# Performance work log

Hardware: AMD Instinct MI355X
Metric: run time of the kernel (lower is better)

Reference implementation:

```python
import jax, jax.numpy as jnp
import numpy as np

N = 50000      # n_nodes
E = 600000     # n_edges (avg degree 12)
IN_DIM = 128
HID = 256
OUT = 2


def _glorot(k, fan_in, fan_out):
    s = jnp.sqrt(6.0 / (fan_in + fan_out))
    return jax.random.uniform(k, (fan_in, fan_out), jnp.float32, -s, s)


def setup_inputs() -> dict:
    key = jax.random.key(0)
    ks = jax.random.split(key, 6)
    x = jax.random.normal(ks[0], (N, IN_DIM), jnp.float32)
    edge_index = jax.random.randint(ks[1], (2, E), 0, N, jnp.int32)
    W1 = _glorot(ks[2], IN_DIM, HID)
    b1 = jnp.zeros((HID,), jnp.float32)
    W2 = _glorot(ks[3], HID, HID)
    b2 = jnp.zeros((HID,), jnp.float32)
    Wl = _glorot(ks[4], HID, OUT)
    bl = jnp.zeros((OUT,), jnp.float32)
    return {"x": x, "edge_index": edge_index, "W1": W1, "b1": b1,
            "W2": W2, "b2": b2, "Wl": Wl, "bl": bl}


def _gcn_conv(x, W, b, src, dst, dinv, n):
    # PyG GCNConv: transform, then propagate with symmetric norm + self-loops.
    h = x @ W                                   # [N, F_out]
    norm = (dinv[src] * dinv[dst])[:, None]     # [E, 1]
    agg = jax.ops.segment_sum(h[src] * norm, dst, num_segments=n)
    agg = agg + h * (dinv * dinv)[:, None]      # self-loop term: deg^-1 * h
    return agg + b


def reference(x, edge_index, W1, b1, W2, b2, Wl, bl):
    n = x.shape[0]
    src, dst = edge_index[0], edge_index[1]
    # degree (with self-loop) computed on destination nodes, as in PyG gcn_norm
    deg = jax.ops.segment_sum(jnp.ones((src.shape[0],), jnp.float32), dst,
                              num_segments=n) + 1.0
    dinv = jax.lax.rsqrt(deg)
    h = jax.nn.relu(_gcn_conv(x, W1, b1, src, dst, dinv, n))
    # dropout is identity in eval mode
    h = jax.nn.relu(_gcn_conv(h, W2, b2, src, dst, dinv, n))
    return h @ Wl + bl
```

## Files before the change

### kernel.cpp

```cpp
#include <hip/hip_runtime.h>
#include <hip/hip_bf16.h>
#include <hip/hip_fp16.h>

constexpr int IN_DIM = 128;
constexpr int HID    = 256;

typedef _Float16 f16x8 __attribute__((ext_vector_type(8)));
typedef float    f32x4 __attribute__((ext_vector_type(4)));


__global__ void count_deg(const int* __restrict__ dst, int* __restrict__ deg, int e) {
    int i = blockIdx.x * blockDim.x + threadIdx.x;
    if (i < e) atomicAdd(&deg[dst[i]], 1);
}

__global__ __launch_bounds__(256) void scan_partial(const int* __restrict__ deg,
                                                    int* __restrict__ escan,
                                                    int* __restrict__ blocksum,
                                                    float* __restrict__ dinv, int n) {
    __shared__ int lds[256];
    int t = threadIdx.x;
    int i = blockIdx.x * 256 + t;
    int v = (i < n) ? deg[i] : 0;
    if (i < n) dinv[i] = rsqrtf((float)v + 1.0f);
    lds[t] = v;
    __syncthreads();
    for (int off = 1; off < 256; off <<= 1) {
        int a = lds[t];
        int w = (t >= off) ? lds[t - off] : 0;
        __syncthreads();
        lds[t] = a + w;
        __syncthreads();
    }
    if (i < n) escan[i] = lds[t] - v;
    if (t == 255) blocksum[blockIdx.x] = lds[255];
}

__global__ __launch_bounds__(256) void scan_rest(const int* __restrict__ escan,
                                                 const int* __restrict__ blocksum,
                                                 int nb, int* __restrict__ rowptr, int n) {
    __shared__ int lds[256];
    int t = threadIdx.x;
    int v = (t < nb) ? blocksum[t] : 0;
    lds[t] = v;
    __syncthreads();
    for (int off = 1; off < 256; off <<= 1) {
        int a = lds[t];
        int w = (t >= off) ? lds[t - off] : 0;
        __syncthreads();
        lds[t] = a + w;
        __syncthreads();
    }
    int boff = (blockIdx.x > 0) ? lds[blockIdx.x - 1] : 0;
    int i = blockIdx.x * 256 + t;
    if (i < n) rowptr[i] = escan[i] + boff;
    if (blockIdx.x == 0 && t == 0) rowptr[n] = lds[nb - 1];
}

__global__ void scatter_edges(const int* __restrict__ src, const int* __restrict__ dst,
                              const int* __restrict__ rowptr, int* __restrict__ cursor,
                              const float* __restrict__ dinv,
                              int2* __restrict__ esw, int e) {
    int i = blockIdx.x * blockDim.x + threadIdx.x;
    if (i < e) {
        int d = dst[i];
        int s = src[i];
        int p = atomicAdd(&cursor[d], 1);
        esw[rowptr[d] + p] = make_int2(s, __float_as_int(dinv[s] * dinv[d]));
    }
}

__device__ inline void conv_B_elem(const float* B, ushort* Bp, int id) {
    int k  = id >> 6;
    int n4 = (id & 63) * 4;
    float4 v = *(const float4*)(B + (size_t)k * 256 + n4);
    size_t base = (size_t)(k >> 5) * (256 * 32) + (k & 31);
    Bp[base + (size_t)(n4 + 0) * 32] = __half_as_ushort(__float2half(v.x));
    Bp[base + (size_t)(n4 + 1) * 32] = __half_as_ushort(__float2half(v.y));
    Bp[base + (size_t)(n4 + 2) * 32] = __half_as_ushort(__float2half(v.z));
    Bp[base + (size_t)(n4 + 3) * 32] = __half_as_ushort(__float2half(v.w));
}

__global__ void convert_inputs(const float* __restrict__ W1, ushort* __restrict__ B1p,
                               const float* __restrict__ W2, ushort* __restrict__ B2p,
                               const float* __restrict__ x, ushort* __restrict__ xh,
                               int total4, int* __restrict__ deg,
                               int* __restrict__ cursor, int n) {
    int id = blockIdx.x * 256 + threadIdx.x;
    constexpr int C1 = IN_DIM * 64;
    constexpr int C2 = C1 + HID * 64;
    if (id < C1) {
        conv_B_elem(W1, B1p, id);
    } else if (id < C2) {
        conv_B_elem(W2, B2p, id - C1);
    } else if (id < C2 + total4) {
        int i = id - C2;
        float4 v = *(const float4*)(x + (size_t)i * 4);
        ushort4 o;
        o.x = __half_as_ushort(__float2half(v.x));
        o.y = __half_as_ushort(__float2half(v.y));
        o.z = __half_as_ushort(__float2half(v.z));
        o.w = __half_as_ushort(__float2half(v.w));
        *(ushort4*)(xh + (size_t)i * 4) = o;
    } else {
        int i = id - (C2 + total4);
        if (i < n) { deg[i] = 0; cursor[i] = 0; }
    }
}

template <int K>
__global__ __launch_bounds__(256) void aggregate_p(const ushort* __restrict__ h,
                                                   const int* __restrict__ rowptr,
                                                   const int2* __restrict__ esw,
                                                   const float* __restrict__ dinv,
                                                   ushort* __restrict__ Pp,
                                                   int n, int Mp) {
    constexpr int VH = K / 64;
    int wid  = (blockIdx.x * 256 + threadIdx.x) >> 6;
    int lane = threadIdx.x & 63;
    if (wid >= n) return;
    float di = dinv[wid];
    float sw = di * di;
    float acc[VH];
    {
        const ushort* row = h + (size_t)wid * K + lane * VH;
        if constexpr (VH == 4) {
            uint2 u = *(const uint2*)row;
            float2 fa = __half22float2(*(__half2*)&u.x);
            float2 fb = __half22float2(*(__half2*)&u.y);
            acc[0] = fa.x * sw; acc[1] = fa.y * sw; acc[2] = fb.x * sw; acc[3] = fb.y * sw;
        } else {
            uint u = *(const uint*)row;
            float2 fa = __half22float2(*(__half2*)&u);
            acc[0] = fa.x * sw; acc[1] = fa.y * sw;
        }
    }
    int beg = rowptr[wid], fin = rowptr[wid + 1];
    for (int b = beg; b < fin; b += 64) {
        int cnt = fin - b;
        if (cnt > 64) cnt = 64;
        int2 pk = (lane < cnt) ? esw[b + lane] : make_int2(0, 0);
        int   sv = pk.x;
        float wv = __int_as_float(pk.y);
        int t = 0;
        for (; t + 8 <= cnt; t += 8) {
            float wr[8];
            if constexpr (VH == 4) {
                uint2 u[8];
#pragma unroll
                for (int k = 0; k < 8; k++) {
                    int s = __shfl(sv, t + k);
                    wr[k] = __shfl(wv, t + k);
                    u[k] = *(const uint2*)(h + (size_t)s * K + lane * VH);
                }
#pragma unroll
                for (int k = 0; k < 8; k++) {
                    float2 fa = __half22float2(*(__half2*)&u[k].x);
                    float2 fb = __half22float2(*(__half2*)&u[k].y);
                    acc[0] += fa.x * wr[k]; acc[1] += fa.y * wr[k];
                    acc[2] += fb.x * wr[k]; acc[3] += fb.y * wr[k];
                }
            } else {
                uint u[8];
#pragma unroll
                for (int k = 0; k < 8; k++) {
                    int s = __shfl(sv, t + k);
                    wr[k] = __shfl(wv, t + k);
                    u[k] = *(const uint*)(h + (size_t)s * K + lane * VH);
                }
#pragma unroll
                for (int k = 0; k < 8; k++) {
                    float2 fa = __half22float2(*(__half2*)&u[k]);
                    acc[0] += fa.x * wr[k]; acc[1] += fa.y * wr[k];
                }
            }
        }
        for (; t + 4 <= cnt; t += 4) {
            float wr[4];
            if constexpr (VH == 4) {
                uint2 u[4];
#pragma unroll
                for (int k = 0; k < 4; k++) {
                    int s = __shfl(sv, t + k);
                    wr[k] = __shfl(wv, t + k);
                    u[k] = *(const uint2*)(h + (size_t)s * K + lane * VH);
                }
#pragma unroll
                for (int k = 0; k < 4; k++) {
                    float2 fa = __half22float2(*(__half2*)&u[k].x);
                    float2 fb = __half22float2(*(__half2*)&u[k].y);
                    acc[0] += fa.x * wr[k]; acc[1] += fa.y * wr[k];
                    acc[2] += fb.x * wr[k]; acc[3] += fb.y * wr[k];
                }
            } else {
                uint u[4];
#pragma unroll
                for (int k = 0; k < 4; k++) {
                    int s = __shfl(sv, t + k);
                    wr[k] = __shfl(wv, t + k);
                    u[k] = *(const uint*)(h + (size_t)s * K + lane * VH);
                }
#pragma unroll
                for (int k = 0; k < 4; k++) {
                    float2 fa = __half22float2(*(__half2*)&u[k]);
                    acc[0] += fa.x * wr[k]; acc[1] += fa.y * wr[k];
                }
            }
        }
        for (; t < cnt; t++) {
            int   s = __shfl(sv, t);
            float w = __shfl(wv, t);
            const ushort* r = h + (size_t)s * K + lane * VH;
            if constexpr (VH == 4) {
                uint2 u = *(const uint2*)r;
                float2 fa = __half22float2(*(__half2*)&u.x);
                float2 fb = __half22float2(*(__half2*)&u.y);
                acc[0] += fa.x * w; acc[1] += fa.y * w;
                acc[2] += fb.x * w; acc[3] += fb.y * w;
            } else {
                uint u = *(const uint*)r;
                float2 fa = __half22float2(*(__half2*)&u);
                acc[0] += fa.x * w; acc[1] += fa.y * w;
            }
        }
    }
    int kglob = lane * VH;
    int chunk = kglob >> 5;
    int inner = kglob & 31;
    size_t base = (size_t)chunk * Mp * 32 + (size_t)wid * 32 + inner;
    if constexpr (VH == 4) {
        __half2 p0 = __floats2half2_rn(acc[0], acc[1]);
        __half2 p1 = __floats2half2_rn(acc[2], acc[3]);
        *(uint2*)&Pp[base] = make_uint2(*(uint*)&p0, *(uint*)&p1);
    } else {
        __half2 p0 = __floats2half2_rn(acc[0], acc[1]);
        *(uint*)&Pp[base] = *(uint*)&p0;
    }
}

template <int K, int MODE>
__global__ __launch_bounds__(256, 3) void gemm_f16(const ushort* __restrict__ Ap,
                                                   const ushort* __restrict__ Bp,
                                                   const float* __restrict__ bias,
                                                   ushort* __restrict__ C16,
                                                   const float* __restrict__ Wl,
                                                   const float* __restrict__ bl,
                                                   float* __restrict__ out,
                                                   int M, int Mp) {
    constexpr int NC = K / 32;
    __shared__ ushort Asm[NC * 1024];
    __shared__ ushort Bsm[2][8192];
    __shared__ float part[4][32][2];

    int tid  = threadIdx.x;
    int w    = tid >> 6;
    int lane = tid & 63;
    int l15  = lane & 15;
    int quad = lane >> 4;
    int row0 = blockIdx.x * 32;

    constexpr int TOTA = NC * 2;
    for (int j = w; j < TOTA; j += 4) {
        int c   = j >> 1;
        int sub = j & 1;
        const ushort* g = Ap + (size_t)c * Mp * 32 + (size_t)(row0 + sub * 16) * 32;
        ushort* l = Asm + c * 1024 + sub * 512;
        __builtin_amdgcn_global_load_lds(
            (const __attribute__((address_space(1))) uint*)(g + (size_t)lane * 8),
            (__attribute__((address_space(3))) uint*)l, 16, 0, 0);
    }
#pragma unroll
    for (int j = 0; j < 4; j++) {
        int seg = w * 4 + j;
        const ushort* g = Bp + (size_t)seg * 512;
        ushort* l = Bsm[0] + seg * 512;
        __builtin_amdgcn_global_load_lds(
            (const __attribute__((address_space(1))) uint*)(g + (size_t)lane * 8),
            (__attribute__((address_space(3))) uint*)l, 16, 0, 0);
    }

    f32x4 acc[2][4] = {};
#pragma unroll
    for (int c = 0; c < NC; c++) {
        __syncthreads();
        if (c + 1 < NC) {
            int nb_ = (c + 1) & 1;
#pragma unroll
            for (int j = 0; j < 4; j++) {
                int seg = w * 4 + j;
                const ushort* g = Bp + (size_t)(c + 1) * 8192 + (size_t)seg * 512;
                ushort* l = Bsm[nb_] + seg * 512;
                __builtin_amdgcn_global_load_lds(
                    (const __attribute__((address_space(1))) uint*)(g + (size_t)lane * 8),
                    (__attribute__((address_space(3))) uint*)l, 16, 0, 0);
            }
        }
        f16x8 fa[2], fb[4];
#pragma unroll
        for (int i = 0; i < 2; i++) {
            int off = c * 1024 + (i * 16 + l15) * 32 + quad * 8;
            fa[i] = *(const f16x8*)&Asm[off];
        }
#pragma unroll
        for (int j = 0; j < 4; j++) {
            int off = (w * 64 + j * 16 + l15) * 32 + quad * 8;
            fb[j] = *(const f16x8*)&Bsm[c & 1][off];
        }
#pragma unroll
        for (int i = 0; i < 2; i++)
#pragma unroll
            for (int j = 0; j < 4; j++)
                acc[i][j] = __builtin_amdgcn_mfma_f32_16x16x32_f16(fa[i], fb[j], acc[i][j], 0, 0, 0);
    }

    float bj[4];
#pragma unroll
    for (int j = 0; j < 4; j++) bj[j] = bias[w * 64 + j * 16 + l15];

    if constexpr (MODE == 1) {
#pragma unroll
        for (int i = 0; i < 2; i++)
#pragma unroll
            for (int reg = 0; reg < 4; reg++) {
                int r = row0 + i * 16 + quad * 4 + reg;
                if (r < M) {
                    ushort* cp = C16 + (size_t)r * 256 + w * 64 + l15;
#pragma unroll
                    for (int j = 0; j < 4; j++) {
                        float v = fmaxf(acc[i][j][reg] + bj[j], 0.f);
                        cp[j * 16] = __half_as_ushort(__float2half(v));
                    }
                }
            }
    } else {
        float wl0[4], wl1[4];
#pragma unroll
        for (int j = 0; j < 4; j++) {
            int cj = w * 64 + j * 16 + l15;
            float2 wv = *(const float2*)(Wl + cj * 2);
            wl0[j] = wv.x; wl1[j] = wv.y;
        }
#pragma unroll
        for (int i = 0; i < 2; i++)
#pragma unroll
            for (int reg = 0; reg < 4; reg++) {
                float s0 = 0.f, s1 = 0.f;
#pragma unroll
                for (int j = 0; j < 4; j++) {
                    float v = fmaxf(acc[i][j][reg] + bj[j], 0.f);
                    s0 += v * wl0[j];
                    s1 += v * wl1[j];
                }
#pragma unroll
                for (int off = 1; off < 16; off <<= 1) {
                    s0 += __shfl_xor(s0, off);
                    s1 += __shfl_xor(s1, off);
                }
                if (l15 == 0) {
                    int r = i * 16 + quad * 4 + reg;
                    part[w][r][0] = s0;
                    part[w][r][1] = s1;
                }
            }
        __syncthreads();
        if (tid < 64) {
            int r = tid >> 1, o = tid & 1;
            int grr = row0 + r;
            if (grr < M) {
                float s = part[0][r][o] + part[1][r][o] + part[2][r][o] + part[3][r][o] + bl[o];
                out[(size_t)grr * 2 + o] = s;
            }
        }
    }
}


extern "C" void kernel_launch(void* const* d_in, const int* in_sizes, int n_in,
                              void* d_out, int out_size, void* d_ws, size_t ws_size,
                              hipStream_t stream) {
    const float* x  = (const float*)d_in[0];
    const int*   ei = (const int*)d_in[1];
    const float* W1 = (const float*)d_in[2];
    const float* b1 = (const float*)d_in[3];
    const float* W2 = (const float*)d_in[4];
    const float* b2 = (const float*)d_in[5];
    const float* Wl = (const float*)d_in[6];
    const float* bl = (const float*)d_in[7];
    float* out = (float*)d_out;

    int n = in_sizes[0] / IN_DIM;
    int e = in_sizes[1] / 2;
    const int* src = ei;
    const int* dst = ei + e;

    int gblocks = (n + 31) / 32;
    int Mp = gblocks * 32;

    char* ws = (char*)d_ws;
    size_t off = 0;
    auto alloc = [&](size_t bytes) -> void* {
        void* p = ws + off;
        off += (bytes + 255) & ~(size_t)255;
        return p;
    };
    int*    deg    = (int*)alloc((size_t)n * 4);
    int*    cursor = (int*)alloc((size_t)n * 4);
    float*  dinv   = (float*)alloc((size_t)n * 4);
    int*    rowptr = (int*)alloc((size_t)(n + 1) * 4);
    int*    escan  = (int*)alloc((size_t)n * 4);
    int*    bsum   = (int*)alloc(256 * 4);
    int2*   esw    = (int2*)alloc((size_t)e * 8);
    ushort* xh     = (ushort*)alloc((size_t)n * IN_DIM * 2);
    ushort* h1     = (ushort*)alloc((size_t)n * HID * 2);
    ushort* A1p    = (ushort*)alloc((size_t)Mp * IN_DIM * 2);
    ushort* A2p    = (ushort*)alloc((size_t)Mp * HID * 2);
    ushort* B1p    = (ushort*)alloc((size_t)IN_DIM * 256 * 2);
    ushort* B2p    = (ushort*)alloc((size_t)HID * 256 * 2);

    int nb = (n + 255) / 256;
    int eb = (e + 255) / 256;

    int total4 = n * IN_DIM / 4;
    int citems = IN_DIM * 64 + HID * 64 + total4 + n;
    convert_inputs<<<(citems + 255) / 256, 256, 0, stream>>>(W1, B1p, W2, B2p, x, xh,
                                                             total4, deg, cursor, n);

    count_deg<<<eb, 256, 0, stream>>>(dst, deg, e);
    scan_partial<<<nb, 256, 0, stream>>>(deg, escan, bsum, dinv, n);
    scan_rest<<<nb, 256, 0, stream>>>(escan, bsum, nb, rowptr, n);
    scatter_edges<<<eb, 256, 0, stream>>>(src, dst, rowptr, cursor, dinv, esw, e);

    aggregate_p<IN_DIM><<<(n + 3) / 4, 256, 0, stream>>>(xh, rowptr, esw, dinv,
                                                         A1p, n, Mp);
    gemm_f16<IN_DIM, 1><<<gblocks, 256, 0, stream>>>(A1p, B1p, b1, h1,
                                                     nullptr, nullptr, nullptr, n, Mp);

    aggregate_p<HID><<<(n + 3) / 4, 256, 0, stream>>>(h1, rowptr, esw, dinv,
                                                      A2p, n, Mp);
    gemm_f16<HID, 2><<<gblocks, 256, 0, stream>>>(A2p, B2p, b2, nullptr,
                                                  Wl, bl, out, n, Mp);
}
```

Before: 251.5 us.

## Fuse neighbor aggregation into GEMM kernel via shared-memory A tile

Merges the per-layer aggregation kernel and the MFMA GEMM kernel into one. Each block aggregates its 32 destination rows (8 per wave) directly into the LDS A tile, so the packed intermediate A1p/A2p buffers are never written to or read back from global memory, and one launch per layer is saved. The LDS A region is reused for the final partial-sum reduction. The trade-off is less parallelism for the irregular gather phase: each wave now walks 8 rows one after another, where before it handled one, and the B prefetch overlaps only with this phase.

```diff
diff --git a/kernel.cpp b/kernel.cpp
--- a/kernel.cpp
+++ b/kernel.cpp
@@ -108,149 +108,22 @@
     }
 }
 
-template <int K>
-__global__ __launch_bounds__(256) void aggregate_p(const ushort* __restrict__ h,
-                                                   const int* __restrict__ rowptr,
-                                                   const int2* __restrict__ esw,
-                                                   const float* __restrict__ dinv,
-                                                   ushort* __restrict__ Pp,
-                                                   int n, int Mp) {
+template <int K, int MODE>
+__global__ __launch_bounds__(256, 3) void fused_layer(const ushort* __restrict__ h,
+                                                      const int* __restrict__ rowptr,
+                                                      const int2* __restrict__ esw,
+                                                      const float* __restrict__ dinv,
+                                                      const ushort* __restrict__ Bp,
+                                                      const float* __restrict__ bias,
+                                                      ushort* __restrict__ C16,
+                                                      const float* __restrict__ Wl,
+                                                      const float* __restrict__ bl,
+                                                      float* __restrict__ out,
+                                                      int M) {
+    constexpr int NC = K / 32;
     constexpr int VH = K / 64;
-    int wid  = (blockIdx.x * 256 + threadIdx.x) >> 6;
-    int lane = threadIdx.x & 63;
-    if (wid >= n) return;
-    float di = dinv[wid];
-    float sw = di * di;
-    float acc[VH];
-    {
-        const ushort* row = h + (size_t)wid * K + lane * VH;
-        if constexpr (VH == 4) {
-            uint2 u = *(const uint2*)row;
-            float2 fa = __half22float2(*(__half2*)&u.x);
-            float2 fb = __half22float2(*(__half2*)&u.y);
-            acc[0] = fa.x * sw; acc[1] = fa.y * sw; acc[2] = fb.x * sw; acc[3] = fb.y * sw;
-        } else {
-            uint u = *(const uint*)row;
-            float2 fa = __half22float2(*(__half2*)&u);
-            acc[0] = fa.x * sw; acc[1] = fa.y * sw;
-        }
-    }
-    int beg = rowptr[wid], fin = rowptr[wid + 1];
-    for (int b = beg; b < fin; b += 64) {
-        int cnt = fin - b;
-        if (cnt > 64) cnt = 64;
-        int2 pk = (lane < cnt) ? esw[b + lane] : make_int2(0, 0);
-        int   sv = pk.x;
-        float wv = __int_as_float(pk.y);
-        int t = 0;
-        for (; t + 8 <= cnt; t += 8) {
-            float wr[8];
-            if constexpr (VH == 4) {
-                uint2 u[8];
-#pragma unroll
-                for (int k = 0; k < 8; k++) {
-                    int s = __shfl(sv, t + k);
-                    wr[k] = __shfl(wv, t + k);
-                    u[k] = *(const uint2*)(h + (size_t)s * K + lane * VH);
-                }
-#pragma unroll
-                for (int k = 0; k < 8; k++) {
-                    float2 fa = __half22float2(*(__half2*)&u[k].x);
-                    float2 fb = __half22float2(*(__half2*)&u[k].y);
-                    acc[0] += fa.x * wr[k]; acc[1] += fa.y * wr[k];
-                    acc[2] += fb.x * wr[k]; acc[3] += fb.y * wr[k];
-                }
-            } else {
-                uint u[8];
-#pragma unroll
-                for (int k = 0; k < 8; k++) {
-                    int s = __shfl(sv, t + k);
-                    wr[k] = __shfl(wv, t + k);
-                    u[k] = *(const uint*)(h + (size_t)s * K + lane * VH);
-                }
-#pragma unroll
-                for (int k = 0; k < 8; k++) {
-                    float2 fa = __half22float2(*(__half2*)&u[k]);
-                    acc[0] += fa.x * wr[k]; acc[1] += fa.y * wr[k];
-                }
-            }
-        }
-        for (; t + 4 <= cnt; t += 4) {
-            float wr[4];
-            if constexpr (VH == 4) {
-                uint2 u[4];
-#pragma unroll
-                for (int k = 0; k < 4; k++) {
-                    int s = __shfl(sv, t + k);
-                    wr[k] = __shfl(wv, t + k);
-                    u[k] = *(const uint2*)(h + (size_t)s * K + lane * VH);
-                }
-#pragma unroll
-                for (int k = 0; k < 4; k++) {
-                    float2 fa = __half22float2(*(__half2*)&u[k].x);
-                    float2 fb = __half22float2(*(__half2*)&u[k].y);
-                    acc[0] += fa.x * wr[k]; acc[1] += fa.y * wr[k];
-                    acc[2] += fb.x * wr[k]; acc[3] += fb.y * wr[k];
-                }
-            } else {
-                uint u[4];
-#pragma unroll
-                for (int k = 0; k < 4; k++) {
-                    int s = __shfl(sv, t + k);
-                    wr[k] = __shfl(wv, t + k);
-                    u[k] = *(const uint*)(h + (size_t)s * K + lane * VH);
-                }
-#pragma unroll
-                for (int k = 0; k < 4; k++) {
-                    float2 fa = __half22float2(*(__half2*)&u[k]);
-                    acc[0] += fa.x * wr[k]; acc[1] += fa.y * wr[k];
-                }
-            }
-        }
-        for (; t < cnt; t++) {
-            int   s = __shfl(sv, t);
-            float w = __shfl(wv, t);
-            const ushort* r = h + (size_t)s * K + lane * VH;
-            if constexpr (VH == 4) {
-                uint2 u = *(const uint2*)r;
-                float2 fa = __half22float2(*(__half2*)&u.x);
-                float2 fb = __half22float2(*(__half2*)&u.y);
-                acc[0] += fa.x * w; acc[1] += fa.y * w;
-                acc[2] += fb.x * w; acc[3] += fb.y * w;
-            } else {
-                uint u = *(const uint*)r;
-                float2 fa = __half22float2(*(__half2*)&u);
-                acc[0] += fa.x * w; acc[1] += fa.y * w;
-            }
-        }
-    }
-    int kglob = lane * VH;
-    int chunk = kglob >> 5;
-    int inner = kglob & 31;
-    size_t base = (size_t)chunk * Mp * 32 + (size_t)wid * 32 + inner;
-    if constexpr (VH == 4) {
-        __half2 p0 = __floats2half2_rn(acc[0], acc[1]);
-        __half2 p1 = __floats2half2_rn(acc[2], acc[3]);
-        *(uint2*)&Pp[base] = make_uint2(*(uint*)&p0, *(uint*)&p1);
-    } else {
-        __half2 p0 = __floats2half2_rn(acc[0], acc[1]);
-        *(uint*)&Pp[base] = *(uint*)&p0;
-    }
-}
-
-template <int K, int MODE>
-__global__ __launch_bounds__(256, 3) void gemm_f16(const ushort* __restrict__ Ap,
-                                                   const ushort* __restrict__ Bp,
-                                                   const float* __restrict__ bias,
-                                                   ushort* __restrict__ C16,
-                                                   const float* __restrict__ Wl,
-                                                   const float* __restrict__ bl,
-                                                   float* __restrict__ out,
-                                                   int M, int Mp) {
-    constexpr int NC = K / 32;
     __shared__ ushort Asm[NC * 1024];
     __shared__ ushort Bsm[2][8192];
-    __shared__ float part[4][32][2];
 
     int tid  = threadIdx.x;
     int w    = tid >> 6;
@@ -259,16 +132,6 @@
     int quad = lane >> 4;
     int row0 = blockIdx.x * 32;
 
-    constexpr int TOTA = NC * 2;
-    for (int j = w; j < TOTA; j += 4) {
-        int c   = j >> 1;
-        int sub = j & 1;
-        const ushort* g = Ap + (size_t)c * Mp * 32 + (size_t)(row0 + sub * 16) * 32;
-        ushort* l = Asm + c * 1024 + sub * 512;
-        __builtin_amdgcn_global_load_lds(
-            (const __attribute__((address_space(1))) uint*)(g + (size_t)lane * 8),
-            (__attribute__((address_space(3))) uint*)l, 16, 0, 0);
-    }
 #pragma unroll
     for (int j = 0; j < 4; j++) {
         int seg = w * 4 + j;
@@ -279,6 +142,130 @@
             (__attribute__((address_space(3))) uint*)l, 16, 0, 0);
     }
 
+    for (int rr = 0; rr < 8; rr++) {
+        int r    = w * 8 + rr;
+        int node = row0 + r;
+        float av[VH];
+#pragma unroll
+        for (int v = 0; v < VH; v++) av[v] = 0.f;
+        if (node < M) {
+            float di = dinv[node];
+            float sw = di * di;
+            const ushort* rowp = h + (size_t)node * K + lane * VH;
+            if constexpr (VH == 4) {
+                uint2 u = *(const uint2*)rowp;
+                float2 fa = __half22float2(*(__half2*)&u.x);
+                float2 fb = __half22float2(*(__half2*)&u.y);
+                av[0] = fa.x * sw; av[1] = fa.y * sw; av[2] = fb.x * sw; av[3] = fb.y * sw;
+            } else {
+                uint u = *(const uint*)rowp;
+                float2 fa = __half22float2(*(__half2*)&u);
+                av[0] = fa.x * sw; av[1] = fa.y * sw;
+            }
+            int beg = rowptr[node], fin = rowptr[node + 1];
+            for (int b = beg; b < fin; b += 64) {
+                int cnt = fin - b;
+                if (cnt > 64) cnt = 64;
+                int2 pk = (lane < cnt) ? esw[b + lane] : make_int2(0, 0);
+                int   sv = pk.x;
+                float wv = __int_as_float(pk.y);
+                int t = 0;
+                for (; t + 8 <= cnt; t += 8) {
+                    float wr[8];
+                    if constexpr (VH == 4) {
+                        uint2 u[8];
+#pragma unroll
+                        for (int k = 0; k < 8; k++) {
+                            int s = __shfl(sv, t + k);
+                            wr[k] = __shfl(wv, t + k);
+                            u[k] = *(const uint2*)(h + (size_t)s * K + lane * VH);
+                        }
+#pragma unroll
+                        for (int k = 0; k < 8; k++) {
+                            float2 fa = __half22float2(*(__half2*)&u[k].x);
+                            float2 fb = __half22float2(*(__half2*)&u[k].y);
+                            av[0] += fa.x * wr[k]; av[1] += fa.y * wr[k];
+                            av[2] += fb.x * wr[k]; av[3] += fb.y * wr[k];
+                        }
+                    } else {
+                        uint u[8];
+#pragma unroll
+                        for (int k = 0; k < 8; k++) {
+                            int s = __shfl(sv, t + k);
+                            wr[k] = __shfl(wv, t + k);
+                            u[k] = *(const uint*)(h + (size_t)s * K + lane * VH);
+                        }
+#pragma unroll
+                        for (int k = 0; k < 8; k++) {
+                            float2 fa = __half22float2(*(__half2*)&u[k]);
+                            av[0] += fa.x * wr[k]; av[1] += fa.y * wr[k];
+                        }
+                    }
+                }
+                for (; t + 4 <= cnt; t += 4) {
+                    float wr[4];
+                    if constexpr (VH == 4) {
+                        uint2 u[4];
+#pragma unroll
+                        for (int k = 0; k < 4; k++) {
+                            int s = __shfl(sv, t + k);
+                            wr[k] = __shfl(wv, t + k);
+                            u[k] = *(const uint2*)(h + (size_t)s * K + lane * VH);
+                        }
+#pragma unroll
+                        for (int k = 0; k < 4; k++) {
+                            float2 fa = __half22float2(*(__half2*)&u[k].x);
+                            float2 fb = __half22float2(*(__half2*)&u[k].y);
+                            av[0] += fa.x * wr[k]; av[1] += fa.y * wr[k];
+                            av[2] += fb.x * wr[k]; av[3] += fb.y * wr[k];
+                        }
+                    } else {
+                        uint u[4];
+#pragma unroll
+                        for (int k = 0; k < 4; k++) {
+                            int s = __shfl(sv, t + k);
+                            wr[k] = __shfl(wv, t + k);
+                            u[k] = *(const uint*)(h + (size_t)s * K + lane * VH);
+                        }
+#pragma unroll
+                        for (int k = 0; k < 4; k++) {
+                            float2 fa = __half22float2(*(__half2*)&u[k]);
+                            av[0] += fa.x * wr[k]; av[1] += fa.y * wr[k];
+                        }
+                    }
+                }
+                for (; t < cnt; t++) {
+                    int   s = __shfl(sv, t);
+                    float wt = __shfl(wv, t);
+                    const ushort* rp = h + (size_t)s * K + lane * VH;
+                    if constexpr (VH == 4) {
+                        uint2 u = *(const uint2*)rp;
+                        float2 fa = __half22float2(*(__half2*)&u.x);
+                        float2 fb = __half22float2(*(__half2*)&u.y);
+                        av[0] += fa.x * wt; av[1] += fa.y * wt;
+                        av[2] += fb.x * wt; av[3] += fb.y * wt;
+                    } else {
+                        uint u = *(const uint*)rp;
+                        float2 fa = __half22float2(*(__half2*)&u);
+                        av[0] += fa.x * wt; av[1] += fa.y * wt;
+                    }
+                }
+            }
+        }
+        if constexpr (VH == 4) {
+            __half2 p0 = __floats2half2_rn(av[0], av[1]);
+            __half2 p1 = __floats2half2_rn(av[2], av[3]);
+            int c = lane >> 3;
+            int inner = (lane & 7) * 4;
+            *(uint2*)&Asm[c * 1024 + r * 32 + inner] = make_uint2(*(uint*)&p0, *(uint*)&p1);
+        } else {
+            __half2 p0 = __floats2half2_rn(av[0], av[1]);
+            int c = lane >> 4;
+            int inner = (lane & 15) * 2;
+            *(uint*)&Asm[c * 1024 + r * 32 + inner] = *(uint*)&p0;
+        }
+    }
+
     f32x4 acc[2][4] = {};
 #pragma unroll
     for (int c = 0; c < NC; c++) {
@@ -333,6 +320,8 @@
                 }
             }
     } else {
+        __syncthreads();
+        float (*part)[32][2] = (float (*)[32][2])Asm;
         float wl0[4], wl1[4];
 #pragma unroll
         for (int j = 0; j < 4; j++) {
@@ -394,7 +383,6 @@
     const int* dst = ei + e;
 
     int gblocks = (n + 31) / 32;
-    int Mp = gblocks * 32;
 
     char* ws = (char*)d_ws;
     size_t off = 0;
@@ -412,8 +400,6 @@
     int2*   esw    = (int2*)alloc((size_t)e * 8);
     ushort* xh     = (ushort*)alloc((size_t)n * IN_DIM * 2);
     ushort* h1     = (ushort*)alloc((size_t)n * HID * 2);
-    ushort* A1p    = (ushort*)alloc((size_t)Mp * IN_DIM * 2);
-    ushort* A2p    = (ushort*)alloc((size_t)Mp * HID * 2);
     ushort* B1p    = (ushort*)alloc((size_t)IN_DIM * 256 * 2);
     ushort* B2p    = (ushort*)alloc((size_t)HID * 256 * 2);
 
@@ -430,13 +416,10 @@
     scan_rest<<<nb, 256, 0, stream>>>(escan, bsum, nb, rowptr, n);
     scatter_edges<<<eb, 256, 0, stream>>>(src, dst, rowptr, cursor, dinv, esw, e);
 
-    aggregate_p<IN_DIM><<<(n + 3) / 4, 256, 0, stream>>>(xh, rowptr, esw, dinv,
-                                                         A1p, n, Mp);
-    gemm_f16<IN_DIM, 1><<<gblocks, 256, 0, stream>>>(A1p, B1p, b1, h1,
-                                                     nullptr, nullptr, nullptr, n, Mp);
-
-    aggregate_p<HID><<<(n + 3) / 4, 256, 0, stream>>>(h1, rowptr, esw, dinv,
-                                                      A2p, n, Mp);
-    gemm_f16<HID, 2><<<gblocks, 256, 0, stream>>>(A2p, B2p, b2, nullptr,
-                                                  Wl, bl, out, n, Mp);
-}
+    fused_layer<IN_DIM, 1><<<gblocks, 256, 0, stream>>>(xh, rowptr, esw, dinv, B1p,
+                                                        b1, h1, nullptr, nullptr,
+                                                        nullptr, n);
+
+    fused_layer<HID, 2><<<gblocks, 256, 0, stream>>>(h1, rowptr, esw, dinv, B2p,
+                                                     b2, nullptr, Wl, bl, out, n);
+}
```

Measured after the change: 273.6 us. 8.8% more time.

## Gather neighbor rows with 16-byte loads split across lane groups in aggregation

Applied to the files above, without the earlier changes.

The aggregation kernel now gives each lane 8 fp16 features through uint4 loads. A row needs only K/8 lanes, so the 64-lane wavefront is split into groups that gather several different neighbor rows at the same time. Partial sums are combined at the end with xor shuffles, and the kernel now sets an occupancy hint of 8 blocks per CU. The aim is wider memory transactions and more loads in flight for the irregular gather, at the cost of extra shuffle reductions and some wasted lanes when a node has few edges.

```diff
diff --git a/kernel.cpp b/kernel.cpp
--- a/kernel.cpp
+++ b/kernel.cpp
@@ -109,32 +109,40 @@
 }
 
 template <int K>
-__global__ __launch_bounds__(256) void aggregate_p(const ushort* __restrict__ h,
-                                                   const int* __restrict__ rowptr,
-                                                   const int2* __restrict__ esw,
-                                                   const float* __restrict__ dinv,
-                                                   ushort* __restrict__ Pp,
-                                                   int n, int Mp) {
-    constexpr int VH = K / 64;
+__global__ __launch_bounds__(256, 8) void aggregate_w(const ushort* __restrict__ h,
+                                                      const int* __restrict__ rowptr,
+                                                      const int2* __restrict__ esw,
+                                                      const float* __restrict__ dinv,
+                                                      ushort* __restrict__ Pp,
+                                                      int n, int Mp) {
+    constexpr int LPR = K / 8;
+    constexpr int R   = 64 / LPR;
+    constexpr int D   = (K == 256) ? 6 : 4;
+
     int wid  = (blockIdx.x * 256 + threadIdx.x) >> 6;
     int lane = threadIdx.x & 63;
     if (wid >= n) return;
+    int g = lane / LPR;
+    int p = lane % LPR;
+
+    float acc[8];
+#pragma unroll
+    for (int i = 0; i < 8; i++) acc[i] = 0.f;
+
     float di = dinv[wid];
-    float sw = di * di;
-    float acc[VH];
-    {
-        const ushort* row = h + (size_t)wid * K + lane * VH;
-        if constexpr (VH == 4) {
-            uint2 u = *(const uint2*)row;
-            float2 fa = __half22float2(*(__half2*)&u.x);
-            float2 fb = __half22float2(*(__half2*)&u.y);
-            acc[0] = fa.x * sw; acc[1] = fa.y * sw; acc[2] = fb.x * sw; acc[3] = fb.y * sw;
-        } else {
-            uint u = *(const uint*)row;
-            float2 fa = __half22float2(*(__half2*)&u);
-            acc[0] = fa.x * sw; acc[1] = fa.y * sw;
-        }
-    }
+    if (g == 0) {
+        float sw = di * di;
+        uint4 u = *(const uint4*)(h + (size_t)wid * K + p * 8);
+        float2 f0 = __half22float2(*(__half2*)&u.x);
+        float2 f1 = __half22float2(*(__half2*)&u.y);
+        float2 f2 = __half22float2(*(__half2*)&u.z);
+        float2 f3 = __half22float2(*(__half2*)&u.w);
+        acc[0] = f0.x * sw; acc[1] = f0.y * sw;
+        acc[2] = f1.x * sw; acc[3] = f1.y * sw;
+        acc[4] = f2.x * sw; acc[5] = f2.y * sw;
+        acc[6] = f3.x * sw; acc[7] = f3.y * sw;
+    }
+
     int beg = rowptr[wid], fin = rowptr[wid + 1];
     for (int b = beg; b < fin; b += 64) {
         int cnt = fin - b;
@@ -142,99 +150,48 @@
         int2 pk = (lane < cnt) ? esw[b + lane] : make_int2(0, 0);
         int   sv = pk.x;
         float wv = __int_as_float(pk.y);
-        int t = 0;
-        for (; t + 8 <= cnt; t += 8) {
-            float wr[8];
-            if constexpr (VH == 4) {
-                uint2 u[8];
-#pragma unroll
-                for (int k = 0; k < 8; k++) {
-                    int s = __shfl(sv, t + k);
-                    wr[k] = __shfl(wv, t + k);
-                    u[k] = *(const uint2*)(h + (size_t)s * K + lane * VH);
-                }
-#pragma unroll
-                for (int k = 0; k < 8; k++) {
-                    float2 fa = __half22float2(*(__half2*)&u[k].x);
-                    float2 fb = __half22float2(*(__half2*)&u[k].y);
-                    acc[0] += fa.x * wr[k]; acc[1] += fa.y * wr[k];
-                    acc[2] += fb.x * wr[k]; acc[3] += fb.y * wr[k];
-                }
-            } else {
-                uint u[8];
-#pragma unroll
-                for (int k = 0; k < 8; k++) {
-                    int s = __shfl(sv, t + k);
-                    wr[k] = __shfl(wv, t + k);
-                    u[k] = *(const uint*)(h + (size_t)s * K + lane * VH);
-                }
-#pragma unroll
-                for (int k = 0; k < 8; k++) {
-                    float2 fa = __half22float2(*(__half2*)&u[k]);
-                    acc[0] += fa.x * wr[k]; acc[1] += fa.y * wr[k];
-                }
-            }
-        }
-        for (; t + 4 <= cnt; t += 4) {
-            float wr[4];
-            if constexpr (VH == 4) {
-                uint2 u[4];
-#pragma unroll
-                for (int k = 0; k < 4; k++) {
-                    int s = __shfl(sv, t + k);
-                    wr[k] = __shfl(wv, t + k);
-                    u[k] = *(const uint2*)(h + (size_t)s * K + lane * VH);
-                }
-#pragma unroll
-                for (int k = 0; k < 4; k++) {
-                    float2 fa = __half22float2(*(__half2*)&u[k].x);
-                    float2 fb = __half22float2(*(__half2*)&u[k].y);
-                    acc[0] += fa.x * wr[k]; acc[1] += fa.y * wr[k];
-                    acc[2] += fb.x * wr[k]; acc[3] += fb.y * wr[k];
-                }
-            } else {
-                uint u[4];
-#pragma unroll
-                for (int k = 0; k < 4; k++) {
-                    int s = __shfl(sv, t + k);
-                    wr[k] = __shfl(wv, t + k);
-                    u[k] = *(const uint*)(h + (size_t)s * K + lane * VH);
-                }
-#pragma unroll
-                for (int k = 0; k < 4; k++) {
-                    float2 fa = __half22float2(*(__half2*)&u[k]);
-                    acc[0] += fa.x * wr[k]; acc[1] += fa.y * wr[k];
-                }
-            }
-        }
-        for (; t < cnt; t++) {
-            int   s = __shfl(sv, t);
-            float w = __shfl(wv, t);
-            const ushort* r = h + (size_t)s * K + lane * VH;
-            if constexpr (VH == 4) {
-                uint2 u = *(const uint2*)r;
-                float2 fa = __half22float2(*(__half2*)&u.x);
-                float2 fb = __half22float2(*(__half2*)&u.y);
-                acc[0] += fa.x * w; acc[1] += fa.y * w;
-                acc[2] += fb.x * w; acc[3] += fb.y * w;
-            } else {
-                uint u = *(const uint*)r;
-                float2 fa = __half22float2(*(__half2*)&u);
-                acc[0] += fa.x * w; acc[1] += fa.y * w;
-            }
-        }
-    }
-    int kglob = lane * VH;
-    int chunk = kglob >> 5;
-    int inner = kglob & 31;
-    size_t base = (size_t)chunk * Mp * 32 + (size_t)wid * 32 + inner;
-    if constexpr (VH == 4) {
-        __half2 p0 = __floats2half2_rn(acc[0], acc[1]);
-        __half2 p1 = __floats2half2_rn(acc[2], acc[3]);
-        *(uint2*)&Pp[base] = make_uint2(*(uint*)&p0, *(uint*)&p1);
-    } else {
-        __half2 p0 = __floats2half2_rn(acc[0], acc[1]);
-        *(uint*)&Pp[base] = *(uint*)&p0;
+        for (int t = 0; t < cnt; t += R * D) {
+            uint4 u[D];
+            float wr[D];
+#pragma unroll
+            for (int k = 0; k < D; k++) {
+                int e  = t + k * R + g;
+                int ee = (e < cnt) ? e : 0;
+                int s   = __shfl(sv, ee);
+                float w = __shfl(wv, ee);
+                wr[k] = (e < cnt) ? w : 0.f;
+                u[k]  = *(const uint4*)(h + (size_t)s * K + p * 8);
+            }
+#pragma unroll
+            for (int k = 0; k < D; k++) {
+                float2 f0 = __half22float2(*(__half2*)&u[k].x);
+                float2 f1 = __half22float2(*(__half2*)&u[k].y);
+                float2 f2 = __half22float2(*(__half2*)&u[k].z);
+                float2 f3 = __half22float2(*(__half2*)&u[k].w);
+                acc[0] += f0.x * wr[k]; acc[1] += f0.y * wr[k];
+                acc[2] += f1.x * wr[k]; acc[3] += f1.y * wr[k];
+                acc[4] += f2.x * wr[k]; acc[5] += f2.y * wr[k];
+                acc[6] += f3.x * wr[k]; acc[7] += f3.y * wr[k];
+            }
+        }
+    }
+
+#pragma unroll
+    for (int i = 0; i < 8; i++) {
+        if constexpr (R == 4) acc[i] += __shfl_xor(acc[i], 16);
+        acc[i] += __shfl_xor(acc[i], 32);
+    }
+
+    if (g == 0) {
+        __half2 q0 = __floats2half2_rn(acc[0], acc[1]);
+        __half2 q1 = __floats2half2_rn(acc[2], acc[3]);
+        __half2 q2 = __floats2half2_rn(acc[4], acc[5]);
+        __half2 q3 = __floats2half2_rn(acc[6], acc[7]);
+        int chunk = p >> 2;
+        int inner = (p & 3) * 8;
+        uint4 o;
+        o.x = *(uint*)&q0; o.y = *(uint*)&q1; o.z = *(uint*)&q2; o.w = *(uint*)&q3;
+        *(uint4*)(Pp + (size_t)chunk * Mp * 32 + (size_t)wid * 32 + inner) = o;
     }
 }
 
@@ -430,12 +387,12 @@
     scan_rest<<<nb, 256, 0, stream>>>(escan, bsum, nb, rowptr, n);
     scatter_edges<<<eb, 256, 0, stream>>>(src, dst, rowptr, cursor, dinv, esw, e);
 
-    aggregate_p<IN_DIM><<<(n + 3) / 4, 256, 0, stream>>>(xh, rowptr, esw, dinv,
+    aggregate_w<IN_DIM><<<(n + 3) / 4, 256, 0, stream>>>(xh, rowptr, esw, dinv,
                                                          A1p, n, Mp);
     gemm_f16<IN_DIM, 1><<<gblocks, 256, 0, stream>>>(A1p, B1p, b1, h1,
                                                      nullptr, nullptr, nullptr, n, Mp);
 
-    aggregate_p<HID><<<(n + 3) / 4, 256, 0, stream>>>(h1, rowptr, esw, dinv,
+    aggregate_w<HID><<<(n + 3) / 4, 256, 0, stream>>>(h1, rowptr, esw, dinv,
                                                       A2p, n, Mp);
     gemm_f16<HID, 2><<<gblocks, 256, 0, stream>>>(A2p, B2p, b2, nullptr,
                                                   Wl, bl, out, n, Mp);
```

Measured after the change: 268.2 us. 1.07x slower.
